# Optimization experiments

Hardware: AMD Instinct MI355X
Metric: run time of the kernel (lower is better)

The kernel has to match this reference:

```python
import jax, jax.numpy as jnp
import numpy as np

T, B = 10, 512
N_ALL, N_AGENTS = 23, 22
N_FEAT = 4
X_DIM = 4
Z_EACH = 4
Z_DIM = N_ALL * Z_EACH  # 92
RNN_H = 64
NH = 8
E = N_ALL * (N_ALL - 1)  # 506

# edge list equivalent of the dense one-hot rel_rec / rel_send matrices
_off = np.ones((N_ALL, N_ALL)) - np.eye(N_ALL)
_recv_np, _send_np = np.where(_off)
RECV = jnp.asarray(_recv_np)  # rel_rec one-hot rows -> receiver node ids
SEND = jnp.asarray(_send_np)  # rel_send one-hot rows -> sender node ids
_et = np.zeros((E, 2), np.float32)
_et[np.arange(0, E, N_ALL - 1)[1:-1], 0] = 1.0
_et[-(N_ALL - 1):, 1] = 1.0
EDGE_TYPE = jnp.asarray(_et)
_nt = np.zeros((N_ALL, 2), np.float32)
_nt[:-1, 0] = 1.0
_nt[-1, 1] = 1.0
NODE_TYPE = jnp.asarray(_nt)


def _bn(x, g, b):
    # BatchNorm1d in training mode over flattened (B*M, C), biased variance
    B_, M, C = x.shape
    xf = x.reshape(B_ * M, C)
    mu = xf.mean(0)
    var = jnp.var(xf, axis=0)
    return ((xf - mu) * jax.lax.rsqrt(var + 1e-5) * g + b).reshape(B_, M, C)


def _mlp(x, W1, b1, W2, b2, g, bt):
    h = jax.nn.elu(jnp.einsum('bmi,hi->bmh', x, W1) + b1)
    h = jax.nn.elu(jnp.einsum('bmi,hi->bmh', h, W2) + b2)
    return _bn(h, g, bt)


def _kld(me, se, mp_, sp):
    return 0.5 * jnp.sum(2.0 * jnp.log(sp / se) + (se ** 2 + (me - mp_) ** 2) / sp ** 2 - 1.0)


def _gru_cell(Wih, Whh, bih, bhh, x, h):
    gi = x @ Wih.T + bih
    gh = h @ Whh.T + bhh
    ir, iz, inn = jnp.split(gi, 3, -1)
    hr, hz, hn = jnp.split(gh, 3, -1)
    r = jax.nn.sigmoid(ir + hr)
    z = jax.nn.sigmoid(iz + hz)
    n = jnp.tanh(inn + r * hn)
    return (1.0 - z) * n + z * h


_gru = jax.vmap(_gru_cell)  # over agents


def _forward(states, eps, mlp1_W1, mlp1_b1, mlp1_W2, mlp1_b2, mlp1_g, mlp1_beta,
             mlp2_W1, mlp2_b1, mlp2_W2, mlp2_b2, mlp2_g, mlp2_beta,
             mlp3_W1, mlp3_b1, mlp3_W2, mlp3_b2, mlp3_g, mlp3_beta,
             enc_mean_W, enc_mean_b, enc_std_W, enc_std_b,
             prior_mean_W, prior_mean_b, prior_std_W, prior_std_b,
             dec_mean_W, dec_mean_b, dec_std_W, dec_std_b,
             gru_Wih, gru_Whh, gru_bih, gru_bhh):
    Bsz = states.shape[2]
    y = states[:T, 0].reshape(T, Bsz, N_ALL, N_FEAT)        # y_t
    x1 = states[1:T + 1, 0].reshape(T, Bsz, N_ALL, N_FEAT)  # x_{t+1}
    P1 = (mlp1_W1, mlp1_b1, mlp1_W2, mlp1_b2, mlp1_g, mlp1_beta)
    P2 = (mlp2_W1, mlp2_b1, mlp2_W2, mlp2_b2, mlp2_g, mlp2_beta)
    P3 = (mlp3_W1, mlp3_b1, mlp3_W2, mlp3_b2, mlp3_g, mlp3_beta)

    def gnn(x, p):
        x = _mlp(x, *(a[p] for a in P1))
        # node2edge: gather senders/receivers instead of one-hot matmul
        e = jnp.concatenate([x[:, SEND], x[:, RECV],
                             jnp.broadcast_to(EDGE_TYPE, (Bsz, E, 2))], -1)
        e = _mlp(e, *(a[p] for a in P2))
        # edge2node: scatter-add into receiver nodes (rel_rec.T @ e)
        inc = jnp.zeros((Bsz, N_ALL, NH), x.dtype).at[:, RECV].add(e)
        inc = jnp.concatenate([inc, jnp.broadcast_to(NODE_TYPE, (Bsz, N_ALL, 2))], -1) / N_ALL
        return _mlp(inc, *(a[p] for a in P3))

    def step(carry, xs):
        h, Lkl = carry
        y_t, x_t, eps_t = xs
        micro = jnp.transpose(h, (1, 0, 2)).reshape(Bsz, -1)  # (B, nA*H)
        pri = jnp.concatenate([gnn(y_t, 0).reshape(Bsz, -1), micro], 1)
        enc = jnp.concatenate([gnn(x_t, 1).reshape(Bsz, -1), micro], 1)
        pm = pri @ prior_mean_W.T + prior_mean_b
        ps = jax.nn.softplus(pri @ prior_std_W.T + prior_std_b)
        em = enc @ enc_mean_W.T + enc_mean_b
        es = jax.nn.softplus(enc @ enc_std_W.T + enc_std_b)
        z = em + es * eps_t  # reparameterized sample_gauss
        Lkl = Lkl + _kld(em, es, pm, ps)
        z_ = z.reshape(Bsz, N_ALL, Z_EACH)
        dg = gnn(z_, 2).reshape(Bsz, -1)
        dm = dg @ dec_mean_W.T + dec_mean_b
        ds = jax.nn.softplus(dg @ dec_std_W.T + dec_std_b)
        # per-agent GRU update: input = [x_t agent feats, z slice]
        gin = jnp.transpose(
            jnp.concatenate([x_t[:, :N_AGENTS, :X_DIM], z_[:, :N_AGENTS]], -1), (1, 0, 2))
        h = _gru(gru_Wih, gru_Whh, gru_bih, gru_bhh, gin, h)
        return (h, Lkl), (dm, ds)

    h0 = jnp.zeros((N_AGENTS, Bsz, RNN_H), states.dtype)
    (_, Lkl), (dms, dss) = jax.lax.scan(step, (h0, jnp.zeros((), states.dtype)), (y, x1, eps))
    return dms, dss, Lkl


def setup_inputs() -> dict:
    key = jax.random.key(0)
    ks = iter(jax.random.split(key, 64))

    def rn(shape, s=0.1):
        return jax.random.normal(next(ks), shape, jnp.float32) * s

    d = {}
    d['states'] = rn((T + 1, 1, B, N_ALL * N_FEAT), 1.0)
    d['eps'] = rn((T, B, Z_DIM), 1.0)
    for i, nin in ((1, N_FEAT), (2, 2 * NH + 2), (3, NH + 2)):
        d['mlp%d_W1' % i] = rn((3, NH, nin), 0.3)
        d['mlp%d_b1' % i] = jnp.full((3, NH), 0.1, jnp.float32)
        d['mlp%d_W2' % i] = rn((3, NH, NH), 0.3)
        d['mlp%d_b2' % i] = jnp.full((3, NH), 0.1, jnp.float32)
        d['mlp%d_g' % i] = jnp.ones((3, NH), jnp.float32)
        d['mlp%d_beta' % i] = jnp.zeros((3, NH), jnp.float32)
    IN_H = NH * N_ALL + RNN_H * N_AGENTS  # 1592
    for nm in ('enc_mean', 'enc_std', 'prior_mean', 'prior_std'):
        d[nm + '_W'] = rn((Z_DIM, IN_H), 0.02)
        d[nm + '_b'] = jnp.zeros((Z_DIM,), jnp.float32)
    OUT_DEC = NH * N_ALL  # 184
    for nm in ('dec_mean', 'dec_std'):
        d[nm + '_W'] = rn((X_DIM * N_AGENTS, OUT_DEC), 0.05)
        d[nm + '_b'] = jnp.zeros((X_DIM * N_AGENTS,), jnp.float32)
    d['gru_Wih'] = rn((N_AGENTS, 3 * RNN_H, X_DIM + Z_EACH), 0.2)
    d['gru_Whh'] = rn((N_AGENTS, 3 * RNN_H, RNN_H), 0.1)
    d['gru_bih'] = jnp.zeros((N_AGENTS, 3 * RNN_H), jnp.float32)
    d['gru_bhh'] = jnp.zeros((N_AGENTS, 3 * RNN_H), jnp.float32)
    return d


def reference(states, eps, mlp1_W1, mlp1_b1, mlp1_W2, mlp1_b2, mlp1_g, mlp1_beta,
              mlp2_W1, mlp2_b1, mlp2_W2, mlp2_b2, mlp2_g, mlp2_beta,
              mlp3_W1, mlp3_b1, mlp3_W2, mlp3_b2, mlp3_g, mlp3_beta,
              enc_mean_W, enc_mean_b, enc_std_W, enc_std_b,
              prior_mean_W, prior_mean_b, prior_std_W, prior_std_b,
              dec_mean_W, dec_mean_b, dec_std_W, dec_std_b,
              gru_Wih, gru_Whh, gru_bih, gru_bhh):
    return _forward(states, eps, mlp1_W1, mlp1_b1, mlp1_W2, mlp1_b2, mlp1_g, mlp1_beta,
                    mlp2_W1, mlp2_b1, mlp2_W2, mlp2_b2, mlp2_g, mlp2_beta,
                    mlp3_W1, mlp3_b1, mlp3_W2, mlp3_b2, mlp3_g, mlp3_beta,
                    enc_mean_W, enc_mean_b, enc_std_W, enc_std_b,
                    prior_mean_W, prior_mean_b, prior_std_W, prior_std_b,
                    dec_mean_W, dec_mean_b, dec_std_W, dec_std_b,
                    gru_Wih, gru_Whh, gru_bih, gru_bhh)
```

## Files before the change

### kernel.cpp

```cpp
#include <hip/hip_runtime.h>
#include <math.h>


__device__ __forceinline__ float elu_(float x){ return x>0.f ? x : __expf(x)-1.f; }
__device__ __forceinline__ float sp_(float x){ return fmaxf(x,0.f)+log1pf(__expf(-fabsf(x))); }
__device__ __forceinline__ float sig_(float x){ return 1.f/(1.f+__expf(-x)); }
__device__ __forceinline__ float wsum_(float v){
  #pragma unroll
  for (int o=32;o;o>>=1) v += __shfl_down(v,o,64);
  return v;
}

__device__ __forceinline__ void reduce_bn_(const float* __restrict__ part, int n,
    float invN, const float* __restrict__ gam, const float* __restrict__ bet,
    float* sc, float* sh, float* tmp)
{
  int tid = threadIdx.x;
  int c = tid & 15, i0 = tid >> 4;
  float s = 0.f;
  for (int i = i0; i < n; i += 16) s += part[i*16 + c];
  tmp[i0*16 + c] = s;
  __syncthreads();
  if (tid < 16){
    float v = 0.f;
    #pragma unroll
    for (int i=0;i<16;i++) v += tmp[i*16 + tid];
    tmp[tid] = v;
  }
  __syncthreads();
  if (tid < 8){
    float m = tmp[tid]*invN;
    float var = tmp[8+tid]*invN - m*m;
    float rs = rsqrtf(var + 1e-5f);
    float s2 = rs*gam[tid];
    sc[tid] = s2; sh[tid] = bet[tid] - m*s2;
  }
  __syncthreads();
}

__device__ __forceinline__ void block_stats_(const float h[8], float* __restrict__ part,
                                             float red[4][16])
{
  int wid = threadIdx.x >> 6, lane = threadIdx.x & 63;
  #pragma unroll
  for (int j=0;j<8;j++){
    float a = wsum_(h[j]);
    float b = wsum_(h[j]*h[j]);
    if (lane==0){ red[wid][j]=a; red[wid][8+j]=b; }
  }
  __syncthreads();
  if (threadIdx.x < 16)
    part[threadIdx.x] = red[0][threadIdx.x]+red[1][threadIdx.x]
                       +red[2][threadIdx.x]+red[3][threadIdx.x];
}


__device__ __forceinline__ void dev_edges(
    float* smem, int b, int g, int p, int t,
    const float* __restrict__ src, long sstride, const float* __restrict__ p1,
    const float* __restrict__ nW1b, const float* __restrict__ nb1b,
    const float* __restrict__ nW2b, const float* __restrict__ nb2b,
    const float* __restrict__ g1b, const float* __restrict__ bt1b,
    const float* __restrict__ eW1b, const float* __restrict__ eb1b,
    const float* __restrict__ eW2b, const float* __restrict__ eb2b,
    float* __restrict__ nodeacc, float* __restrict__ p2)
{
  int tid = threadIdx.x;
  float* tmp   = smem;
  float* sc1   = smem+256;
  float* sh1   = smem+264;
  float* xnode = smem+272;
  float* accs  = smem+480;
  float* redsq = smem+688;
  float* le    = smem+720;
  {
    const float* pp = p1 + (size_t)g*736;
    int c = tid & 15, i0 = tid >> 4;
    float s = 0.f;
    for (int i=i0;i<46;i+=16) s += pp[i*16+c];
    tmp[i0*16+c] = s;
    __syncthreads();
    if (tid<16){
      float v=0.f;
      #pragma unroll
      for (int i=0;i<16;i++) v += tmp[i*16+tid];
      tmp[tid]=v;
    }
    __syncthreads();
    if (tid<8){
      float m = tmp[tid]*(1.f/11776.f);
      float var = tmp[8+tid]*(1.f/11776.f) - m*m;
      float rs = rsqrtf(var+1e-5f);
      float s2 = rs*g1b[p*8+tid];
      sc1[tid]=s2; sh1[tid]=bt1b[p*8+tid]-m*s2;
// ... 34 lines not shown
      #pragma unroll
      for (int j=0;j<8;j++){
        const float* w=W1+j*18;
        float a=b1[j]+w[16]*et0+w[17]*et1;
        #pragma unroll
        for (int k=0;k<8;k++) a+=w[k]*xs[k];
        #pragma unroll
        for (int k=0;k<8;k++) a+=w[8+k]*xr[k];
        h1[j]=elu_(a);
      }
      #pragma unroll
      for (int j=0;j<8;j++){
        float a=b2[j];
        #pragma unroll
        for (int k=0;k<8;k++) a+=W2[j*8+k]*h1[k];
        float h2=elu_(a);
        le[e*9+j]=h2;
        sq[j]+=h2*h2;
      }
    }
  }
  int wid=tid>>6, lane=tid&63;
  #pragma unroll
  for (int j=0;j<8;j++){
    float v=wsum_(sq[j]);
    if (lane==0) redsq[wid*8+j]=v;
  }
  __syncthreads();
  if (tid<184){
    int r=tid>>3, c=tid&7;
    const float* lp = le + r*198 + c;
    float s=0.f;
    #pragma unroll
    for (int jj=0;jj<22;jj++) s+=lp[jj*9];
    accs[r*9+c]=s;
    nodeacc[((size_t)g*512+b)*184+tid]=s;
  }
  __syncthreads();
  if (tid<16){
    int c=tid&7;
    float s=0.f;
    if (tid<8){
      #pragma unroll
      for (int r=0;r<23;r++) s+=accs[r*9+c];
    } else {
      #pragma unroll
      for (int w=0;w<4;w++) s+=redsq[w*8+c];
    }
    p2[((size_t)g*512+b)*16+tid]=s;
  }
}

__device__ __forceinline__ void dev_node3(
    int bi, int g, int p,
    const float* __restrict__ nodeacc, const float* __restrict__ p2,
    const float* __restrict__ g2b, const float* __restrict__ bt2b,
    const float* __restrict__ W3b, const float* __restrict__ b3b,
    const float* __restrict__ W4b, const float* __restrict__ b4b,
    float* __restrict__ out, float* __restrict__ p3)
{
  __shared__ float tmp[256], sc2[8], sh2[8];
  __shared__ float red[4][16];
  reduce_bn_(p2 + (size_t)g*8192, 512, 1.f/259072.f, g2b+p*8, bt2b+p*8, sc2, sh2, tmp);
  int row = bi*256 + threadIdx.x;
  int b = row/23, r = row - b*23;
  const float inv23 = 1.f/23.f;
  const float* na = nodeacc + ((size_t)g*512 + b)*184 + r*8;
  float xk[8];
  #pragma unroll
  for (int k=0;k<8;k++) xk[k] = (na[k]*sc2[k] + 22.f*sh2[k]) * inv23;
  float nt0 = (r<22)?inv23:0.f, nt1 = (r==22)?inv23:0.f;
  const float* W3 = W3b + p*80; const float* b3 = b3b + p*8;
  const float* W4 = W4b + p*64; const float* b4 = b4b + p*8;
  float h1b[8], o[8];
  #pragma unroll
  for (int j=0;j<8;j++){
    const float* w = W3 + j*10;
    float a = b3[j] + w[8]*nt0 + w[9]*nt1;
    #pragma unroll
    for (int k=0;k<8;k++) a += w[k]*xk[k];
    h1b[j] = elu_(a);
  }
  #pragma unroll
  for (int j=0;j<8;j++){
    float a = b4[j];
    #pragma unroll
    for (int k=0;k<8;k++) a += W4[j*8+k]*h1b[k];
    o[j] = elu_(a);
    out[((size_t)g*11776 + row)*8 + j] = o[j];
  }
  block_stats_(o, p3 + ((size_t)g*46 + bi)*16, red);
}

__device__ __forceinline__ void dev_heads(
    float* smem, int idx, int t,
    const float* __restrict__ gy, const float* __restrict__ gx,
    const float* __restrict__ scsh3, const float* __restrict__ h,
    const float* __restrict__ Wpm, const float* __restrict__ Wps,
    const float* __restrict__ Wem, const float* __restrict__ Wes,
    float* __restrict__ rawp)
{
  int bt = idx & 7, head = (idx>>3)&3, kz = idx>>5;
  const float* W  = (head==0)?Wpm:(head==1)?Wps:(head==2)?Wem:Wes;
  const float* gsel = (head<2)?gy:gx;
  int sel = (head<2) ? t : 10+t;
  float* s3 = smem;
  float (*As)[68]  = (float(*)[68])(smem+16);
  float (*Ws)[100] = (float(*)[100])(smem+1104);
  int tid = threadIdx.x;
  if (tid < 16) s3[tid] = scsh3[sel*16 + tid];
  int b0 = bt*64;
  int kbeg = kz*114;
  int kend = kbeg+114; if (kend > 1592) kend = 1592;
  int tb = tid & 15, tj = tid >> 4;
  float acc[4][6];
// ... 4 lines not shown
  __syncthreads();
  for (int k0=kbeg; k0<kend; k0+=16){
    #pragma unroll
    for (int l=0;l<4;l++){
      int lin = tid + 256*l;
      int kk = lin & 15, bl = lin >> 4;
      int i = k0 + kk;
      float v = 0.f;
      if (i < kend){
        int bb = b0 + bl;
        if (i < 184){ int c = i&7; v = gsel[bb*184 + i]*s3[c] + s3[8+c]; }
        else { int i2 = i - 184; v = h[(size_t)(i2>>6)*32768 + bb*64 + (i2&63)]; }
      }
      As[kk][bl] = v;
    }
    #pragma unroll
    for (int l=0;l<6;l++){
      int lin = tid + 256*l;
      int kk = lin & 15, jl = lin >> 4;
      int i = k0 + kk;
      float v = 0.f;
      if (i < kend && jl < 92) v = W[jl*1592 + i];
      Ws[kk][jl] = v;
    }
    __syncthreads();
    #pragma unroll
    for (int kk=0;kk<16;kk++){
      float4 a4 = *(const float4*)&As[kk][tb*4];
      float av[4] = {a4.x,a4.y,a4.z,a4.w};
      float2 w01 = *(const float2*)&Ws[kk][tj*6];
      float2 w23 = *(const float2*)&Ws[kk][tj*6+2];
      float2 w45 = *(const float2*)&Ws[kk][tj*6+4];
      float wv[6] = {w01.x,w01.y,w23.x,w23.y,w45.x,w45.y};
      #pragma unroll
      for (int u=0;u<4;u++)
        #pragma unroll
        for (int vv=0;vv<6;vv++) acc[u][vv] += av[u]*wv[vv];
    }
    __syncthreads();
  }
  float* dst = rawp + (size_t)kz*188416 + (size_t)head*47104;
  #pragma unroll
  for (int u=0;u<4;u++){
    int bb = b0 + tb*4 + u;
    #pragma unroll
    for (int vv=0;vv<6;vv++){
      int j = tj*6 + vv;
      if (j < 92) dst[bb*92 + j] = acc[u][vv];
    }
  }
}

__device__ __forceinline__ void dev_fused(
    int bi,
    const float* __restrict__ rawp,
    const float* __restrict__ bpm, const float* __restrict__ bps,
    const float* __restrict__ bem, const float* __restrict__ bes,
    const float* __restrict__ eps_t, float* __restrict__ z,
    float* __restrict__ lklp,
    const float* __restrict__ W1, const float* __restrict__ b1,
    const float* __restrict__ W2, const float* __restrict__ b2,
    float* __restrict__ part)
{
  __shared__ float redk[4];
  __shared__ float red[4][16];
  int tid = threadIdx.x;
  int row = bi*256 + tid;
  int bb = row/23, n = row - bb*23;
  (void)bb;
  float pm[4]={0,0,0,0}, ps[4]={0,0,0,0}, em[4]={0,0,0,0}, es[4]={0,0,0,0};
  const float* rp = rawp + 4*(size_t)row;
  #pragma unroll
  for (int zz=0;zz<14;zz++){
    const float* q = rp + (size_t)zz*188416;
    float4 a = *(const float4*)(q);
    float4 bq = *(const float4*)(q + 47104);
    float4 c = *(const float4*)(q + 94208);
    float4 d = *(const float4*)(q + 141312);
    pm[0]+=a.x; pm[1]+=a.y; pm[2]+=a.z; pm[3]+=a.w;
    ps[0]+=bq.x; ps[1]+=bq.y; ps[2]+=bq.z; ps[3]+=bq.w;
    em[0]+=c.x; em[1]+=c.y; em[2]+=c.z; em[3]+=c.w;
    es[0]+=d.x; es[1]+=d.y; es[2]+=d.z; es[3]+=d.w;
  }
  int j0 = 4*n;
  float4 e4 = *(const float4*)(eps_t + 4*(size_t)row);
  float ev[4] = {e4.x, e4.y, e4.z, e4.w};
  float zv[4]; float kl = 0.f;
  #pragma unroll
  for (int q=0;q<4;q++){
    float PM = pm[q] + bpm[j0+q];
    float PS = sp_(ps[q] + bps[j0+q]);
    float EM = em[q] + bem[j0+q];
    float ES = sp_(es[q] + bes[j0+q]);
    zv[q] = EM + ES*ev[q];
    float d = EM - PM;
    kl += 0.5f*(2.f*logf(PS/ES) + (ES*ES + d*d)/(PS*PS) - 1.f);
  }
  float4 zq; zq.x=zv[0]; zq.y=zv[1]; zq.z=zv[2]; zq.w=zv[3];
  *(float4*)(z + 4*(size_t)row) = zq;
  float ks = wsum_(kl);
  if ((tid&63)==0) redk[tid>>6] = ks;
  __syncthreads();
  if (tid==0) lklp[bi] = redk[0]+redk[1]+redk[2]+redk[3];
  float h1[8], h2[8];
  #pragma unroll
  for (int j=0;j<8;j++){
    float a = b1[j] + W1[j*4+0]*zv[0] + W1[j*4+1]*zv[1] + W1[j*4+2]*zv[2] + W1[j*4+3]*zv[3];
    h1[j] = elu_(a);
  }
  #pragma unroll
  for (int j=0;j<8;j++){
    float a = b2[j];
    #pragma unroll
    for (int k=0;k<8;k++) a += W2[j*8+k]*h1[k];
    h2[j] = elu_(a);
  }
  block_stats_(h2, part + (size_t)bi*16, red);
}
// ... 76 lines not shown
      float hvv[4] = {hv.x,hv.y,hv.z,hv.w};
      #pragma unroll
      for (int i=0;i<4;i++){ q0[i]+=w0*hvv[i]; q1[i]+=w1*hvv[i]; q2[i]+=w2*hvv[i]; }
    }
    float g0[4], g1[4], g2[4];
    #pragma unroll
    for (int i=0;i<4;i++){ g0[i]=bi0; g1[i]=bi1; g2[i]=bi2; }
    #pragma unroll
    for (int k=0;k<8;k++){
      float4 gv = *(const float4*)&gins[k*36 + s0];
      float gvv[4] = {gv.x,gv.y,gv.z,gv.w};
      #pragma unroll
      for (int i=0;i<4;i++){ g0[i]+=wi0[k]*gvv[i]; g1[i]+=wi1[k]*gvv[i]; g2[i]+=wi2[k]*gvv[i]; }
    }
    float4 hp = *(const float4*)&hs[c*36 + s0];
    float hpv[4] = {hp.x,hp.y,hp.z,hp.w};
    #pragma unroll
    for (int i=0;i<4;i++){
      float rg = sig_(g0[i]+q0[i]);
      float zg = sig_(g1[i]+q1[i]);
      float ng = tanhf(g2[i] + rg*q2[i]);
      h[(size_t)a*32768 + (size_t)(b0+s0+i)*64 + c] = (1.f-zg)*ng + zg*hpv[i];
    }
  }
}


__global__ __launch_bounds__(256) void k_stats1(
    const float* __restrict__ states,
    const float* __restrict__ W1b, const float* __restrict__ b1b,
    const float* __restrict__ W2b, const float* __restrict__ b2b,
    float* __restrict__ part)
{
  int g = blockIdx.y; int p = g/10; int t = g - p*10;
  const float* W1 = W1b + p*32; const float* b1 = b1b + p*8;
  const float* W2 = W2b + p*64; const float* b2 = b2b + p*8;
  int row = blockIdx.x*256 + threadIdx.x;
  float4 x4 = *(const float4*)(states + (size_t)(t+p)*47104 + 4*(size_t)row);
  float h1[8], h2[8];
  #pragma unroll
  for (int j=0;j<8;j++)
    h1[j] = elu_(b1[j] + W1[j*4+0]*x4.x + W1[j*4+1]*x4.y + W1[j*4+2]*x4.z + W1[j*4+3]*x4.w);
  #pragma unroll
  for (int j=0;j<8;j++){
    float a = b2[j];
    #pragma unroll
    for (int k=0;k<8;k++) a += W2[j*8+k]*h1[k];
    h2[j] = elu_(a);
  }
  __shared__ float red[4][16];
  block_stats_(h2, part + ((size_t)g*46 + blockIdx.x)*16, red);
}

__global__ __launch_bounds__(256) void k_pre_edges(
    const float* __restrict__ states, const float* __restrict__ p1,
    const float* __restrict__ nW1, const float* __restrict__ nb1,
    const float* __restrict__ nW2, const float* __restrict__ nb2,
    const float* __restrict__ g1, const float* __restrict__ bt1,
    const float* __restrict__ eW1, const float* __restrict__ eb1,
    const float* __restrict__ eW2, const float* __restrict__ eb2,
    float* __restrict__ nodeacc, float* __restrict__ p2)
{
  __shared__ float smem[5274];
  int g = blockIdx.y, p = g/10, t = g - p*10;
  dev_edges(smem, blockIdx.x, g, p, t, states, 47104L, p1,
            nW1,nb1,nW2,nb2, g1,bt1, eW1,eb1,eW2,eb2, nodeacc, p2);
}

__global__ __launch_bounds__(256) void k_pre_node3(
    const float* __restrict__ nodeacc, const float* __restrict__ p2,
    const float* __restrict__ g2, const float* __restrict__ bt2,
    const float* __restrict__ W3, const float* __restrict__ b3,
    const float* __restrict__ W4, const float* __restrict__ b4,
    float* __restrict__ out, float* __restrict__ p3)
{
  int g = blockIdx.y, p = g/10;
  dev_node3(blockIdx.x, g, p, nodeacc, p2, g2, bt2, W3,b3,W4,b4, out, p3);
}

__global__ __launch_bounds__(256) void k_bnred(
    const float* __restrict__ part, int n, float invN,
    const float* __restrict__ gamb, const float* __restrict__ betb,
    float* __restrict__ scsh)
{
  int g = blockIdx.x; int p = g/10;
  int tid = threadIdx.x;
  __shared__ float tmp[256];
  const float* pp = part + (size_t)g*n*16;
  int c = tid & 15, i0 = tid >> 4;
  float s = 0.f;
  for (int i = i0; i < n; i += 16) s += pp[i*16 + c];
  tmp[i0*16 + c] = s;
  __syncthreads();
  if (tid < 16){
    float v = 0.f;
    #pragma unroll
    for (int i=0;i<16;i++) v += tmp[i*16 + tid];
    tmp[tid] = v;
  }
  __syncthreads();
  if (tid < 8){
    float m = tmp[tid]*invN;
    float var = tmp[8+tid]*invN - m*m;
    float rs = rsqrtf(var + 1e-5f);
    float sc = rs*gamb[p*8+tid];
    scsh[g*16 + tid] = sc;
    scsh[g*16 + 8 + tid] = betb[p*8+tid] - m*sc;
  }
}

__global__ __launch_bounds__(256) void k_K1(
    int nh, int t,
    const float* __restrict__ gy, const float* __restrict__ gx,
    const float* __restrict__ scsh3, const float* __restrict__ h,
    const float* __restrict__ Wpm, const float* __restrict__ Wps,
    const float* __restrict__ Wem, const float* __restrict__ Wes,
    float* __restrict__ rawp,
    const float* __restrict__ zb, const float* __restrict__ zp1,
    const float* __restrict__ nW1, const float* __restrict__ nb1,
    const float* __restrict__ nW2, const float* __restrict__ nb2,
    const float* __restrict__ g1, const float* __restrict__ bt1,
    const float* __restrict__ eW1, const float* __restrict__ eb1,
    const float* __restrict__ eW2, const float* __restrict__ eb2,
    float* __restrict__ zna, float* __restrict__ zp2)
{
  __shared__ float smem[5274];
  if ((int)blockIdx.x < nh)
    dev_heads(smem, blockIdx.x, t, gy, gx, scsh3, h, Wpm,Wps,Wem,Wes, rawp);
  else
    dev_edges(smem, blockIdx.x - nh, 0, 0, 0, zb, 0L, zp1,
              nW1,nb1,nW2,nb2, g1,bt1, eW1,eb1,eW2,eb2, zna, zp2);
}

__global__ __launch_bounds__(256) void k_K2(
    int nf,
    const float* __restrict__ rawp,
    const float* __restrict__ bpm, const float* __restrict__ bps,
    const float* __restrict__ bem, const float* __restrict__ bes,
    const float* __restrict__ eps_t, float* __restrict__ z,
    float* __restrict__ lklp,
    const float* __restrict__ W1, const float* __restrict__ b1,
    const float* __restrict__ W2, const float* __restrict__ b2,
    float* __restrict__ part,
    const float* __restrict__ zna, const float* __restrict__ zp2,
    const float* __restrict__ g2, const float* __restrict__ bt2,
    const float* __restrict__ W3, const float* __restrict__ b3,
    const float* __restrict__ W4, const float* __restrict__ b4,
    float* __restrict__ zg3, float* __restrict__ zp3)
{
  if ((int)blockIdx.x < nf)
    dev_fused(blockIdx.x, rawp, bpm,bps,bem,bes, eps_t, z, lklp, W1,b1,W2,b2, part);
  else
    dev_node3(blockIdx.x - nf, 0, 0, zna, zp2, g2, bt2, W3,b3,W4,b4, zg3, zp3);
}

__global__ __launch_bounds__(256) void k_K3(
    int ngru,
    float* __restrict__ h, const float* __restrict__ x_t,
    const float* __restrict__ z, const float* __restrict__ Wih,
    const float* __restrict__ Whh, const float* __restrict__ bih,
    const float* __restrict__ bhh,
    const float* __restrict__ zg3, const float* __restrict__ p3,
    const float* __restrict__ gam, const float* __restrict__ bet,
    const float* __restrict__ Wm, const float* __restrict__ Bm,
    const float* __restrict__ Wsd, const float* __restrict__ Bsd,
    float* __restrict__ odm, float* __restrict__ ods)
{
  __shared__ float smem[14944];
  if ((int)blockIdx.x < ngru)
    dev_gru(smem, blockIdx.x, h, x_t, z, Wih, Whh, bih, bhh);
  else
    dev_dec(smem, blockIdx.x - ngru, zg3, p3, gam, bet, Wm,Bm,Wsd,Bsd, odm, ods);
}

__global__ __launch_bounds__(256) void k_final(const float* __restrict__ lklp,
                                               float* __restrict__ out){
  __shared__ float red[4];
  float s = 0.f;
  for (int i = threadIdx.x; i < 460; i += 256) s += lklp[i];
  s = wsum_(s);
  if ((threadIdx.x&63)==0) red[threadIdx.x>>6]=s;
  __syncthreads();
  if (threadIdx.x==0) out[0] = red[0]+red[1]+red[2]+red[3];
}

extern "C" void kernel_launch(void* const* d_in, const int* in_sizes, int n_in,
                              void* d_out, int out_size, void* d_ws, size_t ws_size,
                              hipStream_t stream)
{
  (void)in_sizes; (void)n_in; (void)out_size; (void)ws_size;
  const float* states=(const float*)d_in[0];
  const float* eps   =(const float*)d_in[1];
  const float *m1W1=(const float*)d_in[2],  *m1b1=(const float*)d_in[3],
              *m1W2=(const float*)d_in[4],  *m1b2=(const float*)d_in[5],
              *m1g =(const float*)d_in[6],  *m1bt=(const float*)d_in[7];
  const float *m2W1=(const float*)d_in[8],  *m2b1=(const float*)d_in[9],
              *m2W2=(const float*)d_in[10], *m2b2=(const float*)d_in[11],
              *m2g =(const float*)d_in[12], *m2bt=(const float*)d_in[13];
  const float *m3W1=(const float*)d_in[14], *m3b1=(const float*)d_in[15],
              *m3W2=(const float*)d_in[16], *m3b2=(const float*)d_in[17],
              *m3g =(const float*)d_in[18], *m3bt=(const float*)d_in[19];
  const float *emW=(const float*)d_in[20], *emB=(const float*)d_in[21];
  const float *esW=(const float*)d_in[22], *esB=(const float*)d_in[23];
  const float *pmW=(const float*)d_in[24], *pmB=(const float*)d_in[25];
  const float *psW=(const float*)d_in[26], *psB=(const float*)d_in[27];
  const float *dmW=(const float*)d_in[28], *dmB=(const float*)d_in[29];
  const float *dsW=(const float*)d_in[30], *dsB=(const float*)d_in[31];
  const float *gWih=(const float*)d_in[32], *gWhh=(const float*)d_in[33];
  const float *gbih=(const float*)d_in[34], *gbhh=(const float*)d_in[35];
  float* out = (float*)d_out;
  float* ws  = (float*)d_ws;

  float* g3    = ws;
  float* h     = ws + 1884160;
  float* zb    = ws + 2605056;
  float* lklp  = ws + 2652160;
  float* scsh3 = ws + 2652620;
  float* zp1   = ws + 2652940;
  float* zna   = ws + 2653676;
  float* zp2   = ws + 2747884;
  float* zg3   = ws + 2756076;
  float* zp3   = ws + 2850284;
  float* rawp  = ws + 2851020;
  float* p1p = rawp;
  float* naP = rawp + 14720;
  float* p2p = rawp + 1898880;
  float* p3p = rawp + 2062720;

  hipMemsetAsync(h, 0, 720896*sizeof(float), stream);

  k_stats1<<<dim3(46,20),256,0,stream>>>(states, m1W1, m1b1, m1W2, m1b2, p1p);
  k_pre_edges<<<dim3(512,20),256,0,stream>>>(states, p1p,
      m1W1, m1b1, m1W2, m1b2, m1g, m1bt,
      m2W1, m2b1, m2W2, m2b2, naP, p2p);
  k_pre_node3<<<dim3(46,20),256,0,stream>>>(naP, p2p, m2g, m2bt,
      m3W1, m3b1, m3W2, m3b2, g3, p3p);
  k_bnred<<<20,256,0,stream>>>(p3p, 46, 1.f/11776.f, m3g, m3bt, scsh3);

  for (int t=0;t<=10;t++){
    int nh = (t<10)?448:0, ne = (t>0)?512:0;
    k_K1<<<nh+ne,256,0,stream>>>(nh, t,
        g3 + (size_t)(t<10?t:0)*94208, g3 + 942080 + (size_t)(t<10?t:0)*94208,
        scsh3, h, pmW, psW, emW, esW, rawp,
        zb, zp1,
        m1W1+64, m1b1+16, m1W2+128, m1b2+16, m1g+16, m1bt+16,
        m2W1+288, m2b1+16, m2W2+128, m2b2+16, zna, zp2);
    int nf = (t<10)?46:0, nn = (t>0)?46:0;
    k_K2<<<nf+nn,256,0,stream>>>(nf,
        rawp, pmB, psB, emB, esB,
        eps + (size_t)(t<10?t:0)*47104, zb, lklp + (t<10?t:0)*46,
        m1W1+64, m1b1+16, m1W2+128, m1b2+16, zp1,
        zna, zp2, m2g+16, m2bt+16,
        m3W1+160, m3b1+16, m3W2+128, m3b2+16, zg3, zp3);
    int ng = (t<10)?352:0, nd = (t>0)?352:0;
    float* odm = (t>0) ? out + (size_t)(t-1)*45056 : out;
    float* ods = (t>0) ? out + 450560 + (size_t)(t-1)*45056 : out;
    k_K3<<<ng+nd,256,0,stream>>>(ng,
        h, states + (size_t)(t<10?t+1:1)*47104, zb, gWih, gWhh, gbih, gbhh,
        zg3, zp3, m3g+16, m3bt+16, dmW, dmB, dsW, dsB, odm, ods);
  }
  k_final<<<1,256,0,stream>>>(lklp, out + 901120);
}
```

Baseline: 852.4 us.

## Fuse time-step loop into one cooperative persistent kernel with grid syncs

Replaces the 33 per-timestep kernel launches plus the final reduction kernel with a single cooperative kernel. It loops over timesteps and phases, uses grid.sync between phases, and strides blocks over the work items. Separately, k_pre_edges is rewritten to use 512 threads per block so that one thread handles each of the 506 edges, with its BN-stat reduction inlined. This removes launch gaps and kernel boundaries, at the cost of grid-wide barriers and a grid capped by occupancy, which may serialize larger phases.

Measured after the change: 2.268 ms. 166% more time.

```diff
diff --git a/kernel.cpp b/kernel.cpp
--- a/kernel.cpp
+++ b/kernel.cpp
@@ -1,5 +1,8 @@
 #include <hip/hip_runtime.h>
+#include <hip/hip_cooperative_groups.h>
 #include <math.h>
+
+namespace cg = cooperative_groups;
 
 
 __device__ __forceinline__ float elu_(float x){ return x>0.f ? x : __expf(x)-1.f; }
@@ -39,7 +42,7 @@
 }
 
 __device__ __forceinline__ void block_stats_(const float h[8], float* __restrict__ part,
-                                             float red[4][16])
+                                             float red[][16])
 {
   int wid = threadIdx.x >> 6, lane = threadIdx.x & 63;
   #pragma unroll
@@ -180,15 +183,15 @@
 }
 
 __device__ __forceinline__ void dev_node3(
-    int bi, int g, int p,
+    float* smem, int bi, int g, int p,
     const float* __restrict__ nodeacc, const float* __restrict__ p2,
     const float* __restrict__ g2b, const float* __restrict__ bt2b,
     const float* __restrict__ W3b, const float* __restrict__ b3b,
     const float* __restrict__ W4b, const float* __restrict__ b4b,
     float* __restrict__ out, float* __restrict__ p3)
 {
-  __shared__ float tmp[256], sc2[8], sh2[8];
-  __shared__ float red[4][16];
+  float* tmp = smem; float* sc2 = smem+256; float* sh2 = smem+264;
+  float (*red)[16] = (float(*)[16])(smem+272);
   reduce_bn_(p2 + (size_t)g*8192, 512, 1.f/259072.f, g2b+p*8, bt2b+p*8, sc2, sh2, tmp);
   int row = bi*256 + threadIdx.x;
   int b = row/23, r = row - b*23;
@@ -299,7 +302,7 @@
 }
 
 __device__ __forceinline__ void dev_fused(
-    int bi,
+    float* smem, int bi,
     const float* __restrict__ rawp,
     const float* __restrict__ bpm, const float* __restrict__ bps,
     const float* __restrict__ bem, const float* __restrict__ bes,
@@ -309,8 +312,8 @@
     const float* __restrict__ W2, const float* __restrict__ b2,
     float* __restrict__ part)
 {
-  __shared__ float redk[4];
-  __shared__ float red[4][16];
+  float* redk = smem;
+  float (*red)[16] = (float(*)[16])(smem+4);
   int tid = threadIdx.x;
   int row = bi*256 + tid;
   int bb = row/23, n = row - bb*23;
@@ -493,19 +496,122 @@
   block_stats_(h2, part + ((size_t)g*46 + blockIdx.x)*16, red);
 }
 
-__global__ __launch_bounds__(256) void k_pre_edges(
-    const float* __restrict__ states, const float* __restrict__ p1,
-    const float* __restrict__ nW1, const float* __restrict__ nb1,
-    const float* __restrict__ nW2, const float* __restrict__ nb2,
-    const float* __restrict__ g1, const float* __restrict__ bt1,
-    const float* __restrict__ eW1, const float* __restrict__ eb1,
-    const float* __restrict__ eW2, const float* __restrict__ eb2,
+__global__ __launch_bounds__(512) void k_pre_edges(
+    const float* __restrict__ src, const float* __restrict__ p1,
+    const float* __restrict__ nW1b, const float* __restrict__ nb1b,
+    const float* __restrict__ nW2b, const float* __restrict__ nb2b,
+    const float* __restrict__ g1b, const float* __restrict__ bt1b,
+    const float* __restrict__ eW1b, const float* __restrict__ eb1b,
+    const float* __restrict__ eW2b, const float* __restrict__ eb2b,
     float* __restrict__ nodeacc, float* __restrict__ p2)
 {
-  __shared__ float smem[5274];
-  int g = blockIdx.y, p = g/10, t = g - p*10;
-  dev_edges(smem, blockIdx.x, g, p, t, states, 47104L, p1,
-            nW1,nb1,nW2,nb2, g1,bt1, eW1,eb1,eW2,eb2, nodeacc, p2);
+  int g = blockIdx.y; int p = g/10; int t = g - p*10; int b = blockIdx.x;
+  int tid = threadIdx.x;
+  __shared__ float tmp[512];
+  __shared__ float sc1[8], sh1[8];
+  __shared__ float xnode[207];
+  __shared__ float le[4554];
+  __shared__ float accs[207];
+  __shared__ float redsq[8][8];
+  {
+    const float* pp = p1 + (size_t)g*736;
+    int c = tid & 15, i0 = tid >> 4;
+    float s = 0.f;
+    for (int i = i0; i < 46; i += 32) s += pp[i*16 + c];
+    tmp[i0*16 + c] = s;
+    __syncthreads();
+    if (tid < 16){
+      float v = 0.f;
+      #pragma unroll
+      for (int i=0;i<32;i++) v += tmp[i*16 + tid];
+      tmp[tid] = v;
+    }
+    __syncthreads();
+    if (tid < 8){
+      float m = tmp[tid]*(1.f/11776.f);
+      float var = tmp[8+tid]*(1.f/11776.f) - m*m;
+      float rs = rsqrtf(var + 1e-5f);
+      float s2 = rs*g1b[p*8+tid];
+      sc1[tid] = s2; sh1[tid] = bt1b[p*8+tid] - m*s2;
+    }
+    __syncthreads();
+  }
+  if (tid < 23){
+    const float* x = src + (size_t)(t+p)*47104 + (size_t)b*92 + tid*4;
+    const float* W1 = nW1b + p*32; const float* b1 = nb1b + p*8;
+    const float* W2 = nW2b + p*64; const float* b2 = nb2b + p*8;
+    float x0=x[0], x1=x[1], x2=x[2], x3=x[3];
+    float h1[8];
+    #pragma unroll
+    for (int j=0;j<8;j++)
+      h1[j] = elu_(b1[j] + W1[j*4]*x0 + W1[j*4+1]*x1 + W1[j*4+2]*x2 + W1[j*4+3]*x3);
+    #pragma unroll
+    for (int j=0;j<8;j++){
+      float a = b2[j];
+      #pragma unroll
+      for (int k=0;k<8;k++) a += W2[j*8+k]*h1[k];
+      xnode[tid*9+j] = elu_(a)*sc1[j] + sh1[j];
+    }
+  }
+  __syncthreads();
+  float sq[8] = {0,0,0,0,0,0,0,0};
+  if (tid < 506){
+    int r = tid/22, jj = tid - r*22;
+    int s = jj + (jj>=r ? 1 : 0);
+    const float* W1 = eW1b + p*144; const float* b1 = eb1b + p*8;
+    const float* W2 = eW2b + p*64;  const float* b2 = eb2b + p*8;
+    float et0 = (jj==0 && r>=1 && r<=21) ? 1.f : 0.f;
+    float et1 = (r==22) ? 1.f : 0.f;
+    float h1[8];
+    #pragma unroll
+    for (int j=0;j<8;j++){
+      const float* w = W1 + j*18;
+      float a = b1[j] + w[16]*et0 + w[17]*et1;
+      #pragma unroll
+      for (int k=0;k<8;k++) a += w[k]*xnode[s*9+k];
+      #pragma unroll
+      for (int k=0;k<8;k++) a += w[8+k]*xnode[r*9+k];
+      h1[j] = elu_(a);
+    }
+    #pragma unroll
+    for (int j=0;j<8;j++){
+      float a = b2[j];
+      #pragma unroll
+      for (int k=0;k<8;k++) a += W2[j*8+k]*h1[k];
+      float h2 = elu_(a);
+      le[tid*9+j] = h2;
+      sq[j] = h2*h2;
+    }
+  }
+  int wid = tid >> 6, lane = tid & 63;
+  #pragma unroll
+  for (int j=0;j<8;j++){
+    float v = wsum_(sq[j]);
+    if (lane==0) redsq[wid][j] = v;
+  }
+  __syncthreads();
+  if (tid < 184){
+    int r = tid >> 3, c = tid & 7;
+    const float* lp = le + r*198 + c;
+    float s = 0.f;
+    #pragma unroll
+    for (int jj=0;jj<22;jj++) s += lp[jj*9];
+    accs[r*9+c] = s;
+    nodeacc[((size_t)g*512 + b)*184 + tid] = s;
+  }
+  __syncthreads();
+  if (tid < 16){
+    int c = tid & 7;
+    float s = 0.f;
+    if (tid < 8){
+      #pragma unroll
+      for (int r=0;r<23;r++) s += accs[r*9+c];
+    } else {
+      #pragma unroll
+      for (int w=0;w<8;w++) s += redsq[w][c];
+    }
+    p2[((size_t)g*512 + b)*16 + tid] = s;
+  }
 }
 
 __global__ __launch_bounds__(256) void k_pre_node3(
@@ -515,8 +621,9 @@
     const float* __restrict__ W4, const float* __restrict__ b4,
     float* __restrict__ out, float* __restrict__ p3)
 {
+  __shared__ float smem[336];
   int g = blockIdx.y, p = g/10;
-  dev_node3(blockIdx.x, g, p, nodeacc, p2, g2, bt2, W3,b3,W4,b4, out, p3);
+  dev_node3(smem, blockIdx.x, g, p, nodeacc, p2, g2, bt2, W3,b3,W4,b4, out, p3);
 }
 
 __global__ __launch_bounds__(256) void k_bnred(
@@ -550,79 +657,70 @@
   }
 }
 
-__global__ __launch_bounds__(256) void k_K1(
-    int nh, int t,
-    const float* __restrict__ gy, const float* __restrict__ gx,
-    const float* __restrict__ scsh3, const float* __restrict__ h,
-    const float* __restrict__ Wpm, const float* __restrict__ Wps,
-    const float* __restrict__ Wem, const float* __restrict__ Wes,
-    float* __restrict__ rawp,
-    const float* __restrict__ zb, const float* __restrict__ zp1,
-    const float* __restrict__ nW1, const float* __restrict__ nb1,
-    const float* __restrict__ nW2, const float* __restrict__ nb2,
-    const float* __restrict__ g1, const float* __restrict__ bt1,
-    const float* __restrict__ eW1, const float* __restrict__ eb1,
-    const float* __restrict__ eW2, const float* __restrict__ eb2,
-    float* __restrict__ zna, float* __restrict__ zp2)
-{
-  __shared__ float smem[5274];
-  if ((int)blockIdx.x < nh)
-    dev_heads(smem, blockIdx.x, t, gy, gx, scsh3, h, Wpm,Wps,Wem,Wes, rawp);
-  else
-    dev_edges(smem, blockIdx.x - nh, 0, 0, 0, zb, 0L, zp1,
-              nW1,nb1,nW2,nb2, g1,bt1, eW1,eb1,eW2,eb2, zna, zp2);
-}
-
-__global__ __launch_bounds__(256) void k_K2(
-    int nf,
-    const float* __restrict__ rawp,
-    const float* __restrict__ bpm, const float* __restrict__ bps,
-    const float* __restrict__ bem, const float* __restrict__ bes,
-    const float* __restrict__ eps_t, float* __restrict__ z,
-    float* __restrict__ lklp,
-    const float* __restrict__ W1, const float* __restrict__ b1,
-    const float* __restrict__ W2, const float* __restrict__ b2,
-    float* __restrict__ part,
-    const float* __restrict__ zna, const float* __restrict__ zp2,
-    const float* __restrict__ g2, const float* __restrict__ bt2,
-    const float* __restrict__ W3, const float* __restrict__ b3,
-    const float* __restrict__ W4, const float* __restrict__ b4,
-    float* __restrict__ zg3, float* __restrict__ zp3)
-{
-  if ((int)blockIdx.x < nf)
-    dev_fused(blockIdx.x, rawp, bpm,bps,bem,bes, eps_t, z, lklp, W1,b1,W2,b2, part);
-  else
-    dev_node3(blockIdx.x - nf, 0, 0, zna, zp2, g2, bt2, W3,b3,W4,b4, zg3, zp3);
-}
-
-__global__ __launch_bounds__(256) void k_K3(
-    int ngru,
-    float* __restrict__ h, const float* __restrict__ x_t,
-    const float* __restrict__ z, const float* __restrict__ Wih,
-    const float* __restrict__ Whh, const float* __restrict__ bih,
-    const float* __restrict__ bhh,
-    const float* __restrict__ zg3, const float* __restrict__ p3,
-    const float* __restrict__ gam, const float* __restrict__ bet,
-    const float* __restrict__ Wm, const float* __restrict__ Bm,
-    const float* __restrict__ Wsd, const float* __restrict__ Bsd,
-    float* __restrict__ odm, float* __restrict__ ods)
-{
+
+struct SArgs {
+  const float *states, *eps;
+  const float *m1W1,*m1b1,*m1W2,*m1b2,*m1g,*m1bt;
+  const float *m2W1,*m2b1,*m2W2,*m2b2,*m2g,*m2bt;
+  const float *m3W1,*m3b1,*m3W2,*m3b2,*m3g,*m3bt;
+  const float *emB,*esB,*pmW,*pmB,*psW,*psB,*emW,*esW;
+  const float *dmW,*dmB,*dsW,*dsB;
+  const float *gWih,*gWhh,*gbih,*gbhh;
+  float *out;
+  float *h,*g3,*zb,*lklp,*scsh3,*zp1,*zna,*zp2,*zg3,*zp3,*rawp;
+};
+
+__global__ __launch_bounds__(256,2) void k_scan(SArgs A)
+{
+  cg::grid_group grid = cg::this_grid();
   __shared__ float smem[14944];
-  if ((int)blockIdx.x < ngru)
-    dev_gru(smem, blockIdx.x, h, x_t, z, Wih, Whh, bih, bhh);
-  else
-    dev_dec(smem, blockIdx.x - ngru, zg3, p3, gam, bet, Wm,Bm,Wsd,Bsd, odm, ods);
-}
-
-__global__ __launch_bounds__(256) void k_final(const float* __restrict__ lklp,
-                                               float* __restrict__ out){
-  __shared__ float red[4];
-  float s = 0.f;
-  for (int i = threadIdx.x; i < 460; i += 256) s += lklp[i];
-  s = wsum_(s);
-  if ((threadIdx.x&63)==0) red[threadIdx.x>>6]=s;
-  __syncthreads();
-  if (threadIdx.x==0) out[0] = red[0]+red[1]+red[2]+red[3];
+  const int NB = gridDim.x;
+  for (int t=0;t<=10;t++){
+    int nh = (t<10)?448:0, ne = (t>0)?512:0;
+    for (int it = blockIdx.x; it < nh+ne; it += NB){
+      __syncthreads();
+      if (it < nh)
+        dev_heads(smem, it, t, A.g3 + (size_t)t*94208, A.g3 + 942080 + (size_t)t*94208,
+                  A.scsh3, A.h, A.pmW, A.psW, A.emW, A.esW, A.rawp);
+      else
+        dev_edges(smem, it - nh, 0, 0, 0, A.zb, 0L, A.zp1,
+                  A.m1W1+64, A.m1b1+16, A.m1W2+128, A.m1b2+16, A.m1g+16, A.m1bt+16,
+                  A.m2W1+288, A.m2b1+16, A.m2W2+128, A.m2b2+16, A.zna, A.zp2);
+    }
+    grid.sync();
+    int nf = (t<10)?46:0, nn = (t>0)?46:0;
+    for (int it = blockIdx.x; it < nf+nn; it += NB){
+      __syncthreads();
+      if (it < nf)
+        dev_fused(smem, it, A.rawp, A.pmB, A.psB, A.emB, A.esB,
+                  A.eps + (size_t)t*47104, A.zb, A.lklp + t*46,
+                  A.m1W1+64, A.m1b1+16, A.m1W2+128, A.m1b2+16, A.zp1);
+      else
+        dev_node3(smem, it - nf, 0, 0, A.zna, A.zp2, A.m2g+16, A.m2bt+16,
+                  A.m3W1+160, A.m3b1+16, A.m3W2+128, A.m3b2+16, A.zg3, A.zp3);
+    }
+    grid.sync();
+    int ng = (t<10)?352:0, nd = (t>0)?352:0;
+    for (int it = blockIdx.x; it < ng+nd; it += NB){
+      __syncthreads();
+      if (it < ng)
+        dev_gru(smem, it, A.h, A.states + (size_t)(t+1)*47104, A.zb,
+                A.gWih, A.gWhh, A.gbih, A.gbhh);
+      else
+        dev_dec(smem, it - ng, A.zg3, A.zp3, A.m3g+16, A.m3bt+16,
+                A.dmW, A.dmB, A.dsW, A.dsB,
+                A.out + (size_t)(t-1)*45056, A.out + 450560 + (size_t)(t-1)*45056);
+    }
+    grid.sync();
+  }
+  if (blockIdx.x == 0){
+    float s = 0.f;
+    for (int i = threadIdx.x; i < 460; i += 256) s += A.lklp[i];
+    s = wsum_(s);
+    if ((threadIdx.x&63)==0) smem[threadIdx.x>>6] = s;
+    __syncthreads();
+    if (threadIdx.x==0) A.out[901120] = smem[0]+smem[1]+smem[2]+smem[3];
+  }
 }
 
 extern "C" void kernel_launch(void* const* d_in, const int* in_sizes, int n_in,
@@ -671,34 +769,32 @@
   hipMemsetAsync(h, 0, 720896*sizeof(float), stream);
 
   k_stats1<<<dim3(46,20),256,0,stream>>>(states, m1W1, m1b1, m1W2, m1b2, p1p);
-  k_pre_edges<<<dim3(512,20),256,0,stream>>>(states, p1p,
+  k_pre_edges<<<dim3(512,20),512,0,stream>>>(states, p1p,
       m1W1, m1b1, m1W2, m1b2, m1g, m1bt,
       m2W1, m2b1, m2W2, m2b2, naP, p2p);
   k_pre_node3<<<dim3(46,20),256,0,stream>>>(naP, p2p, m2g, m2bt,
       m3W1, m3b1, m3W2, m3b2, g3, p3p);
   k_bnred<<<20,256,0,stream>>>(p3p, 46, 1.f/11776.f, m3g, m3bt, scsh3);
 
-  for (int t=0;t<=10;t++){
-    int nh = (t<10)?448:0, ne = (t>0)?512:0;
-    k_K1<<<nh+ne,256,0,stream>>>(nh, t,
-        g3 + (size_t)(t<10?t:0)*94208, g3 + 942080 + (size_t)(t<10?t:0)*94208,
-        scsh3, h, pmW, psW, emW, esW, rawp,
-        zb, zp1,
-        m1W1+64, m1b1+16, m1W2+128, m1b2+16, m1g+16, m1bt+16,
-        m2W1+288, m2b1+16, m2W2+128, m2b2+16, zna, zp2);
-    int nf = (t<10)?46:0, nn = (t>0)?46:0;
-    k_K2<<<nf+nn,256,0,stream>>>(nf,
-        rawp, pmB, psB, emB, esB,
-        eps + (size_t)(t<10?t:0)*47104, zb, lklp + (t<10?t:0)*46,
-        m1W1+64, m1b1+16, m1W2+128, m1b2+16, zp1,
-        zna, zp2, m2g+16, m2bt+16,
-        m3W1+160, m3b1+16, m3W2+128, m3b2+16, zg3, zp3);
-    int ng = (t<10)?352:0, nd = (t>0)?352:0;
-    float* odm = (t>0) ? out + (size_t)(t-1)*45056 : out;
-    float* ods = (t>0) ? out + 450560 + (size_t)(t-1)*45056 : out;
-    k_K3<<<ng+nd,256,0,stream>>>(ng,
-        h, states + (size_t)(t<10?t+1:1)*47104, zb, gWih, gWhh, gbih, gbhh,
-        zg3, zp3, m3g+16, m3bt+16, dmW, dmB, dsW, dsB, odm, ods);
-  }
-  k_final<<<1,256,0,stream>>>(lklp, out + 901120);
-}
+  int maxb = 0;
+  hipOccupancyMaxActiveBlocksPerMultiprocessor(&maxb, k_scan, 256, 0);
+  if (maxb < 1) maxb = 1;
+  int grid = maxb * 256;
+  if (grid > 960) grid = 960;
+
+  SArgs sa;
+  sa.states=states; sa.eps=eps;
+  sa.m1W1=m1W1; sa.m1b1=m1b1; sa.m1W2=m1W2; sa.m1b2=m1b2; sa.m1g=m1g; sa.m1bt=m1bt;
+  sa.m2W1=m2W1; sa.m2b1=m2b1; sa.m2W2=m2W2; sa.m2b2=m2b2; sa.m2g=m2g; sa.m2bt=m2bt;
+  sa.m3W1=m3W1; sa.m3b1=m3b1; sa.m3W2=m3W2; sa.m3b2=m3b2; sa.m3g=m3g; sa.m3bt=m3bt;
+  sa.emB=emB; sa.esB=esB; sa.pmW=pmW; sa.pmB=pmB; sa.psW=psW; sa.psB=psB;
+  sa.emW=emW; sa.esW=esW;
+  sa.dmW=dmW; sa.dmB=dmB; sa.dsW=dsW; sa.dsB=dsB;
+  sa.gWih=gWih; sa.gWhh=gWhh; sa.gbih=gbih; sa.gbhh=gbhh;
+  sa.out=out;
+  sa.h=h; sa.g3=g3; sa.zb=zb; sa.lklp=lklp; sa.scsh3=scsh3;
+  sa.zp1=zp1; sa.zna=zna; sa.zp2=zp2; sa.zg3=zg3; sa.zp3=zp3; sa.rawp=rawp;
+
+  void* kargs[] = { (void*)&sa };
+  hipLaunchCooperativeKernel((void*)k_scan, dim3(grid), dim3(256), kargs, 0, stream);
+}
```

## Rewrite pre-pass edge kernel with one thread per edge at 512 threads

Applied to the files above, without the earlier changes.

The precompute edge kernel is reimplemented to use 512 threads per block. Each block first reduces the BN1 partial stats, then computes the 23 node embeddings, then has one thread per edge (506 edges) evaluate the edge MLP, and finally reduces the per-receiver sums and squared stats in shared memory. Shared memory in the fused K2 path is also made explicit rather than declared inside the device function. This aims to cut serial per-thread work in the one-time prepass, at the cost of higher shared memory and register pressure per block.

Result: faster. 820.6 us (-3.7%).

```diff
diff --git a/kernel.cpp b/kernel.cpp
--- a/kernel.cpp
+++ b/kernel.cpp
@@ -39,7 +39,7 @@
 }
 
 __device__ __forceinline__ void block_stats_(const float h[8], float* __restrict__ part,
-                                             float red[4][16])
+                                             float red[][16])
 {
   int wid = threadIdx.x >> 6, lane = threadIdx.x & 63;
   #pragma unroll
@@ -299,7 +299,7 @@
 }
 
 __device__ __forceinline__ void dev_fused(
-    int bi,
+    float* smem, int bi,
     const float* __restrict__ rawp,
     const float* __restrict__ bpm, const float* __restrict__ bps,
     const float* __restrict__ bem, const float* __restrict__ bes,
@@ -309,8 +309,8 @@
     const float* __restrict__ W2, const float* __restrict__ b2,
     float* __restrict__ part)
 {
-  __shared__ float redk[4];
-  __shared__ float red[4][16];
+  float* redk = smem;
+  float (*red)[16] = (float(*)[16])(smem+4);
   int tid = threadIdx.x;
   int row = bi*256 + tid;
   int bb = row/23, n = row - bb*23;
@@ -493,19 +493,122 @@
   block_stats_(h2, part + ((size_t)g*46 + blockIdx.x)*16, red);
 }
 
-__global__ __launch_bounds__(256) void k_pre_edges(
-    const float* __restrict__ states, const float* __restrict__ p1,
-    const float* __restrict__ nW1, const float* __restrict__ nb1,
-    const float* __restrict__ nW2, const float* __restrict__ nb2,
-    const float* __restrict__ g1, const float* __restrict__ bt1,
-    const float* __restrict__ eW1, const float* __restrict__ eb1,
-    const float* __restrict__ eW2, const float* __restrict__ eb2,
+__global__ __launch_bounds__(512) void k_pre_edges(
+    const float* __restrict__ src, const float* __restrict__ p1,
+    const float* __restrict__ nW1b, const float* __restrict__ nb1b,
+    const float* __restrict__ nW2b, const float* __restrict__ nb2b,
+    const float* __restrict__ g1b, const float* __restrict__ bt1b,
+    const float* __restrict__ eW1b, const float* __restrict__ eb1b,
+    const float* __restrict__ eW2b, const float* __restrict__ eb2b,
     float* __restrict__ nodeacc, float* __restrict__ p2)
 {
-  __shared__ float smem[5274];
-  int g = blockIdx.y, p = g/10, t = g - p*10;
-  dev_edges(smem, blockIdx.x, g, p, t, states, 47104L, p1,
-            nW1,nb1,nW2,nb2, g1,bt1, eW1,eb1,eW2,eb2, nodeacc, p2);
+  int g = blockIdx.y; int p = g/10; int t = g - p*10; int b = blockIdx.x;
+  int tid = threadIdx.x;
+  __shared__ float tmp[512];
+  __shared__ float sc1[8], sh1[8];
+  __shared__ float xnode[207];
+  __shared__ float le[4554];
+  __shared__ float accs[207];
+  __shared__ float redsq[8][8];
+  {
+    const float* pp = p1 + (size_t)g*736;
+    int c = tid & 15, i0 = tid >> 4;
+    float s = 0.f;
+    for (int i = i0; i < 46; i += 32) s += pp[i*16 + c];
+    tmp[i0*16 + c] = s;
+    __syncthreads();
+    if (tid < 16){
+      float v = 0.f;
+      #pragma unroll
+      for (int i=0;i<32;i++) v += tmp[i*16 + tid];
+      tmp[tid] = v;
+    }
+    __syncthreads();
+    if (tid < 8){
+      float m = tmp[tid]*(1.f/11776.f);
+      float var = tmp[8+tid]*(1.f/11776.f) - m*m;
+      float rs = rsqrtf(var + 1e-5f);
+      float s2 = rs*g1b[p*8+tid];
+      sc1[tid] = s2; sh1[tid] = bt1b[p*8+tid] - m*s2;
+    }
+    __syncthreads();
+  }
+  if (tid < 23){
+    const float* x = src + (size_t)(t+p)*47104 + (size_t)b*92 + tid*4;
+    const float* W1 = nW1b + p*32; const float* b1 = nb1b + p*8;
+    const float* W2 = nW2b + p*64; const float* b2 = nb2b + p*8;
+    float x0=x[0], x1=x[1], x2=x[2], x3=x[3];
+    float h1[8];
+    #pragma unroll
+    for (int j=0;j<8;j++)
+      h1[j] = elu_(b1[j] + W1[j*4]*x0 + W1[j*4+1]*x1 + W1[j*4+2]*x2 + W1[j*4+3]*x3);
+    #pragma unroll
+    for (int j=0;j<8;j++){
+      float a = b2[j];
+      #pragma unroll
+      for (int k=0;k<8;k++) a += W2[j*8+k]*h1[k];
+      xnode[tid*9+j] = elu_(a)*sc1[j] + sh1[j];
+    }
+  }
+  __syncthreads();
+  float sq[8] = {0,0,0,0,0,0,0,0};
+  if (tid < 506){
+    int r = tid/22, jj = tid - r*22;
+    int s = jj + (jj>=r ? 1 : 0);
+    const float* W1 = eW1b + p*144; const float* b1 = eb1b + p*8;
+    const float* W2 = eW2b + p*64;  const float* b2 = eb2b + p*8;
+    float et0 = (jj==0 && r>=1 && r<=21) ? 1.f : 0.f;
+    float et1 = (r==22) ? 1.f : 0.f;
+    float h1[8];
+    #pragma unroll
+    for (int j=0;j<8;j++){
+      const float* w = W1 + j*18;
+      float a = b1[j] + w[16]*et0 + w[17]*et1;
+      #pragma unroll
+      for (int k=0;k<8;k++) a += w[k]*xnode[s*9+k];
+      #pragma unroll
+      for (int k=0;k<8;k++) a += w[8+k]*xnode[r*9+k];
+      h1[j] = elu_(a);
+    }
+    #pragma unroll
+    for (int j=0;j<8;j++){
+      float a = b2[j];
+      #pragma unroll
+      for (int k=0;k<8;k++) a += W2[j*8+k]*h1[k];
+      float h2 = elu_(a);
+      le[tid*9+j] = h2;
+      sq[j] = h2*h2;
+    }
+  }
+  int wid = tid >> 6, lane = tid & 63;
+  #pragma unroll
+  for (int j=0;j<8;j++){
+    float v = wsum_(sq[j]);
+    if (lane==0) redsq[wid][j] = v;
+  }
+  __syncthreads();
+  if (tid < 184){
+    int r = tid >> 3, c = tid & 7;
+    const float* lp = le + r*198 + c;
+    float s = 0.f;
+    #pragma unroll
+    for (int jj=0;jj<22;jj++) s += lp[jj*9];
+    accs[r*9+c] = s;
+    nodeacc[((size_t)g*512 + b)*184 + tid] = s;
+  }
+  __syncthreads();
+  if (tid < 16){
+    int c = tid & 7;
+    float s = 0.f;
+    if (tid < 8){
+      #pragma unroll
+      for (int r=0;r<23;r++) s += accs[r*9+c];
+    } else {
+      #pragma unroll
+      for (int w=0;w<8;w++) s += redsq[w][c];
+    }
+    p2[((size_t)g*512 + b)*16 + tid] = s;
+  }
 }
 
 __global__ __launch_bounds__(256) void k_pre_node3(
@@ -549,6 +652,7 @@
     scsh[g*16 + 8 + tid] = betb[p*8+tid] - m*sc;
   }
 }
+
 
 __global__ __launch_bounds__(256) void k_K1(
     int nh, int t,
@@ -589,8 +693,9 @@
     const float* __restrict__ W4, const float* __restrict__ b4,
     float* __restrict__ zg3, float* __restrict__ zp3)
 {
+  __shared__ float smem[68];
   if ((int)blockIdx.x < nf)
-    dev_fused(blockIdx.x, rawp, bpm,bps,bem,bes, eps_t, z, lklp, W1,b1,W2,b2, part);
+    dev_fused(smem, blockIdx.x, rawp, bpm,bps,bem,bes, eps_t, z, lklp, W1,b1,W2,b2, part);
   else
     dev_node3(blockIdx.x - nf, 0, 0, zna, zp2, g2, bt2, W3,b3,W4,b4, zg3, zp3);
 }
@@ -671,7 +776,7 @@
   hipMemsetAsync(h, 0, 720896*sizeof(float), stream);
 
   k_stats1<<<dim3(46,20),256,0,stream>>>(states, m1W1, m1b1, m1W2, m1b2, p1p);
-  k_pre_edges<<<dim3(512,20),256,0,stream>>>(states, p1p,
+  k_pre_edges<<<dim3(512,20),512,0,stream>>>(states, p1p,
       m1W1, m1b1, m1W2, m1b2, m1g, m1bt,
       m2W1, m2b1, m2W2, m2b2, naP, p2p);
   k_pre_node3<<<dim3(46,20),256,0,stream>>>(naP, p2p, m2g, m2bt,
@@ -680,25 +785,29 @@
 
   for (int t=0;t<=10;t++){
     int nh = (t<10)?448:0, ne = (t>0)?512:0;
-    k_K1<<<nh+ne,256,0,stream>>>(nh, t,
-        g3 + (size_t)(t<10?t:0)*94208, g3 + 942080 + (size_t)(t<10?t:0)*94208,
-        scsh3, h, pmW, psW, emW, esW, rawp,
-        zb, zp1,
-        m1W1+64, m1b1+16, m1W2+128, m1b2+16, m1g+16, m1bt+16,
-        m2W1+288, m2b1+16, m2W2+128, m2b2+16, zna, zp2);
+    int tt = (t<10)? t : 0;
+    if (nh+ne > 0)
+      k_K1<<<nh+ne,256,0,stream>>>(nh, tt,
+          g3 + (size_t)tt*94208, g3 + 942080 + (size_t)tt*94208,
+          scsh3, h, pmW, psW, emW, esW, rawp,
+          zb, zp1,
+          m1W1+64, m1b1+16, m1W2+128, m1b2+16, m1g+16, m1bt+16,
+          m2W1+288, m2b1+16, m2W2+128, m2b2+16, zna, zp2);
     int nf = (t<10)?46:0, nn = (t>0)?46:0;
-    k_K2<<<nf+nn,256,0,stream>>>(nf,
-        rawp, pmB, psB, emB, esB,
-        eps + (size_t)(t<10?t:0)*47104, zb, lklp + (t<10?t:0)*46,
-        m1W1+64, m1b1+16, m1W2+128, m1b2+16, zp1,
-        zna, zp2, m2g+16, m2bt+16,
-        m3W1+160, m3b1+16, m3W2+128, m3b2+16, zg3, zp3);
+    if (nf+nn > 0)
+      k_K2<<<nf+nn,256,0,stream>>>(nf,
+          rawp, pmB, psB, emB, esB,
+          eps + (size_t)tt*47104, zb, lklp + tt*46,
+          m1W1+64, m1b1+16, m1W2+128, m1b2+16, zp1,
+          zna, zp2, m2g+16, m2bt+16,
+          m3W1+160, m3b1+16, m3W2+128, m3b2+16, zg3, zp3);
     int ng = (t<10)?352:0, nd = (t>0)?352:0;
-    float* odm = (t>0) ? out + (size_t)(t-1)*45056 : out;
-    float* ods = (t>0) ? out + 450560 + (size_t)(t-1)*45056 : out;
-    k_K3<<<ng+nd,256,0,stream>>>(ng,
-        h, states + (size_t)(t<10?t+1:1)*47104, zb, gWih, gWhh, gbih, gbhh,
-        zg3, zp3, m3g+16, m3bt+16, dmW, dmB, dsW, dsB, odm, ods);
+    int tm1 = (t>0)? t-1 : 0;
+    if (ng+nd > 0)
+      k_K3<<<ng+nd,256,0,stream>>>(ng,
+          h, states + (size_t)(tt+1)*47104, zb, gWih, gWhh, gbih, gbhh,
+          zg3, zp3, m3g+16, m3bt+16, dmW, dmB, dsW, dsB,
+          out + (size_t)tm1*45056, out + 450560 + (size_t)tm1*45056);
   }
   k_final<<<1,256,0,stream>>>(lklp, out + 901120);
 }
```
